# Performance work log

Measured on AMD Instinct MI355X. Metric: run time of the kernel, lower is better.

Reference implementation:

```python
import jax, jax.numpy as jnp
import numpy as np

B, T, D = 2, 2048, 1024
H = 16
HD = D // H  # head dim == config.k == config.v == 64


def setup_inputs() -> dict:
    key = jax.random.key(0)
    k1, k2, k3 = jax.random.split(key, 3)
    scale = 0.02
    x = jax.random.normal(k1, (B, T, D), dtype=jnp.float32)
    W1 = jax.random.normal(k2, (D, 3 * D), dtype=jnp.float32) * scale
    b1 = jnp.zeros((3 * D,), dtype=jnp.float32)
    W2 = jax.random.normal(k3, (D, D), dtype=jnp.float32) * scale
    b2 = jnp.zeros((D,), dtype=jnp.float32)
    return {"x": x, "W1": W1, "b1": b1, "W2": W2, "b2": b2}


def reference(x, W1, b1, W2, b2):
    # Fused QKV projection (dropout layers are identity in eval mode).
    Bx, Tx, C = x.shape
    qkv = x @ W1 + b1                      # [B, T, 3D]
    q, k, v = jnp.split(qkv, 3, axis=-1)   # each [B, T, D]
    q = q.reshape(Bx, Tx, H, HD).transpose(0, 2, 1, 3)  # [B, H, T, hd]
    k = k.reshape(Bx, Tx, H, HD).transpose(0, 2, 1, 3)
    v = v.reshape(Bx, Tx, H, HD).transpose(0, 2, 1, 3)

    logits = jnp.einsum('bhmk,bhnk->bhmn', q, k) / jnp.sqrt(jnp.float32(HD))
    # causal mask (lower-triangular bias buffer)
    causal = jnp.tril(jnp.ones((Tx, Tx), dtype=bool))
    logits = jnp.where(causal[None, None], logits, jnp.float32(-jnp.inf))
    att = jax.nn.softmax(logits, axis=-1)   # [B, H, T, T]

    y = jnp.einsum('bhmn,bhnv->bhmv', att, v)        # [B, H, T, hd]
    y = y.transpose(0, 2, 1, 3).reshape(Bx, Tx, C)   # [B, T, D]
    return y @ W2 + b2
```

## Files before the change

### kernel.cpp

```cpp
#include <hip/hip_runtime.h>

typedef __attribute__((ext_vector_type(8))) short bf16x8;
typedef __attribute__((ext_vector_type(4))) float f32x4;
typedef __attribute__((ext_vector_type(16))) float f32x16;
typedef __attribute__((ext_vector_type(4))) short short4v;
typedef __attribute__((ext_vector_type(4))) unsigned int uint4v;

#define B_  2
#define T_  2048
#define D_  1024
#define H_  16
#define HD_ 64

__device__ inline short f2bf(float f){
  unsigned u = __builtin_bit_cast(unsigned, f);
  u += 0x7fff + ((u >> 16) & 1);
  return (short)(u >> 16);
}

__device__ inline void gl2lds16(const void* g, void* l){
  __builtin_amdgcn_global_load_lds(
      (const __attribute__((address_space(1))) unsigned int*)g,
      (__attribute__((address_space(3))) unsigned int*)l, 16, 0, 0);
}

__global__ __launch_bounds__(256) void convert_f32_bf16(
    const float* __restrict__ in, short* __restrict__ out){
  int i = (blockIdx.x * 256 + threadIdx.x) * 4;
  float4 v = *(const float4*)(in + i);
  short4v o;
  o[0] = f2bf(v.x); o[1] = f2bf(v.y); o[2] = f2bf(v.z); o[3] = f2bf(v.w);
  *(short4v*)(out + i) = o;
}

__global__ __launch_bounds__(256) void transpose_f32_bf16(
    const float* __restrict__ in, short* __restrict__ out, int R, int C){
  __shared__ float tile[32][33];
  int tx = threadIdx.x & 31, ty0 = threadIdx.x >> 5;
  int bx = blockIdx.x << 5, by = blockIdx.y << 5;
#pragma unroll
  for (int i = 0; i < 4; i++){
    int ty = ty0 + i * 8;
    tile[ty][tx] = in[(by + ty) * C + bx + tx];
  }
  __syncthreads();
#pragma unroll
  for (int i = 0; i < 4; i++){
    int ty = ty0 + i * 8;
    out[(bx + ty) * R + by + tx] = f2bf(tile[tx][ty]);
  }
}

#define BM 128
#define BN 128
#define BK 32

#define QSCALE 0.18033688011112042f

template<int N_, int K_, int EPI>
__global__ __launch_bounds__(256) void gemm_bt(
    const short* __restrict__ A, const short* __restrict__ Bt,
    const float* __restrict__ bias,
    short* __restrict__ q, short* __restrict__ kk, short* __restrict__ vT,
    float* __restrict__ outf){
  __shared__ short As[2][BM * BK];
  __shared__ short Bs[2][BN * BK];
  const int tid = threadIdx.x;
  const int lane = tid & 63, w = tid >> 6;
  const int wm = w >> 1, wn = w & 1;
  const int lr = lane & 15, lk = lane >> 4;
  const int brow = blockIdx.y * BM, bcol = blockIdx.x * BN;
  f32x4 acc[4][4] = {};
  const short* Ag = A  + brow * K_;
  const short* Bg = Bt + bcol * K_;

  auto stage = [&](int buf, int k0){
#pragma unroll
    for (int i = 0; i < 2; i++){
      int idx = i * 256 + tid;
      int row = idx >> 2, c8 = (idx & 3) * 8;
      gl2lds16(Ag + row * K_ + k0 + c8, (char*)As[buf] + idx * 16);
      gl2lds16(Bg + row * K_ + k0 + c8, (char*)Bs[buf] + idx * 16);
    }
  };

  const int NT = K_ / BK;
  stage(0, 0);
  for (int t = 0; t < NT; ++t){
    const int cur = t & 1;
    if (t + 1 < NT){
      stage(cur ^ 1, (t + 1) * BK);
      asm volatile("s_waitcnt vmcnt(4)" ::: "memory");
    } else {
      asm volatile("s_waitcnt vmcnt(0)" ::: "memory");
    }
    __builtin_amdgcn_s_barrier();
    __builtin_amdgcn_sched_barrier(0);

    bf16x8 a[4], b[4];
#pragma unroll
    for (int mf = 0; mf < 4; mf++)
      a[mf] = *(const bf16x8*)(As[cur] + (wm * 64 + mf * 16 + lr) * BK + lk * 8);
#pragma unroll
    for (int nf = 0; nf < 4; nf++)
      b[nf] = *(const bf16x8*)(Bs[cur] + (wn * 64 + nf * 16 + lr) * BK + lk * 8);
    __builtin_amdgcn_s_setprio(1);
#pragma unroll
    for (int mf = 0; mf < 4; mf++)
#pragma unroll
      for (int nf = 0; nf < 4; nf++)
        acc[mf][nf] = __builtin_amdgcn_mfma_f32_16x16x32_bf16(a[mf], b[nf], acc[mf][nf], 0, 0, 0);
    __builtin_amdgcn_s_setprio(0);
    __builtin_amdgcn_sched_barrier(0);
    __builtin_amdgcn_s_barrier();
  }

  if constexpr (EPI == 0){
#pragma unroll
    for (int nf = 0; nf < 4; nf++){
      int n = bcol + wn * 64 + nf * 16 + lr;
      float bv = bias[n];
      int sec = n >> 10, d = n & 1023, h = d >> 6, hd = d & 63;
#pragma unroll
      for (int mf = 0; mf < 4; mf++){
        int m0 = brow + wm * 64 + mf * 16 + lk * 4;
        int b = m0 >> 11, t0 = m0 & 2047;
        int bh = b * H_ + h;
        if (sec == 0){
#pragma unroll
          for (int r = 0; r < 4; r++)
            q[(bh * T_ + t0 + r) * HD_ + hd] = f2bf((acc[mf][nf][r] + bv) * QSCALE);
        } else if (sec == 1){
#pragma unroll
          for (int r = 0; r < 4; r++)
            kk[(bh * T_ + t0 + r) * HD_ + hd] = f2bf(acc[mf][nf][r] + bv);
        } else {
          float v0 = acc[mf][nf][0] + bv, v1 = acc[mf][nf][1] + bv;
          float v2 = acc[mf][nf][2] + bv, v3 = acc[mf][nf][3] + bv;
          unsigned lo = (unsigned)(unsigned short)f2bf(v0) | ((unsigned)(unsigned short)f2bf(v1) << 16);
          unsigned hi = (unsigned)(unsigned short)f2bf(v2) | ((unsigned)(unsigned short)f2bf(v3) << 16);
          uint2 pk; pk.x = lo; pk.y = hi;
          *(uint2*)(vT + (bh * HD_ + hd) * T_ + t0) = pk;
        }
      }
    }
  } else {
#pragma unroll
    for (int nf = 0; nf < 4; nf++){
      int n = bcol + wn * 64 + nf * 16 + lr;
      float bv = bias[n];
#pragma unroll
      for (int mf = 0; mf < 4; mf++){
        int m0 = brow + wm * 64 + mf * 16 + lk * 4;
#pragma unroll
        for (int r = 0; r < 4; r++)
          outf[(m0 + r) * N_ + n] = acc[mf][nf][r] + bv;
      }
    }
  }
}

__global__ __launch_bounds__(256) void attn32(
    const short* __restrict__ Q, const short* __restrict__ Kg,
    const short* __restrict__ Vt, short* __restrict__ Y){
  __shared__ short Ks[2][64 * 64];
  __shared__ short Vs[2][64 * 64];
  __shared__ float bounce[4][32];
  const int tid = threadIdx.x;
  const int w = tid >> 6, l = tid & 63;
  const int lq = l & 31, h = l >> 5;
  const int bx = blockIdx.x;
  const int i = (bx < 256) ? 15 - (bx >> 5) : (bx >> 5) - 8;
  const int bh = bx & 31;
  const int q0 = i * 128, qw = q0 + w * 32;
  const int nt = 2 * (i + 1);

  bf16x8 qb[4];
  {
    const short* qbase = Q + (bh * T_ + qw + lq) * HD_;
#pragma unroll
    for (int dk = 0; dk < 4; dk++)
      qb[dk] = *(const bf16x8*)(qbase + dk * 16 + h * 8);
  }

  f32x16 o0 = {}, o1 = {};
  float m = -1e30f, ll = 0.f;

  auto stage = [&](int buf, int t){
#pragma unroll
    for (int j = 0; j < 2; j++){
      int idx = j * 256 + tid;
      int row = idx >> 3, cb = (idx & 7) * 16;
      int cbs = cb ^ ((row & 7) << 4);
      gl2lds16(Kg + (bh * T_ + t * 64 + row) * HD_ + (cbs >> 1), (char*)Ks[buf] + idx * 16);
      gl2lds16(Vt + (bh * HD_ + row) * T_ + t * 64 + (cbs >> 1), (char*)Vs[buf] + idx * 16);
    }
  };

  stage(0, 0);
  for (int t = 0; t < nt; ++t){
    const int cur = t & 1;
    if (t + 1 < nt){
      stage(cur ^ 1, t + 1);
      asm volatile("s_waitcnt vmcnt(4)" ::: "memory");
    } else {
      asm volatile("s_waitcnt vmcnt(0)" ::: "memory");
    }
    __builtin_amdgcn_s_barrier();
    __builtin_amdgcn_sched_barrier(0);

    const int kvb = t * 64;
    if (kvb <= qw + 31){
      const short* Kc = Ks[cur];
      const short* Vc = Vs[cur];

      f32x16 s[2] = {};
      __builtin_amdgcn_s_setprio(1);
#pragma unroll
      for (int kb = 0; kb < 2; kb++){
        int row = kb * 32 + lq;
        const char* rp = (const char*)Kc + row * 128;
        int swz = (row & 7) << 4;
#pragma unroll
        for (int dk = 0; dk < 4; dk++){
          bf16x8 ka = *(const bf16x8*)(rp + ((dk * 32 + h * 16) ^ swz));
          s[kb] = __builtin_amdgcn_mfma_f32_32x32x16_bf16(ka, qb[dk], s[kb], 0, 0, 0);
        }
      }
      __builtin_amdgcn_s_setprio(0);

      const int qg = qw + lq;
      if (kvb + 63 > qw){
#pragma unroll
        for (int kb = 0; kb < 2; kb++)
#pragma unroll
          for (int r = 0; r < 16; r++){
            int kv = kvb + kb * 32 + (r & 3) + 8 * (r >> 2) + 4 * h;
            if (kv > qg) s[kb][r] = -1e30f;
          }
      }

      float pm = s[0][0];
#pragma unroll
      for (int r = 1; r < 16; r++) pm = fmaxf(pm, s[0][r]);
#pragma unroll
      for (int r = 0; r < 16; r++) pm = fmaxf(pm, s[1][r]);
      pm = fmaxf(pm, __shfl_xor(pm, 32));

      if (__any(pm > m + 8.f)){
        float mn = fmaxf(pm, m);
        float sf = __builtin_amdgcn_exp2f(m - mn);
        m = mn;
        ll *= sf;
        bounce[w][lq] = sf;
#pragma unroll
        for (int r = 0; r < 16; r++){
          float sr = bounce[w][(r & 3) + 8 * (r >> 2) + 4 * h];
          o0[r] *= sr; o1[r] *= sr;
        }
      }

      float ts = 0.f;
#pragma unroll
      for (int kb = 0; kb < 2; kb++)
#pragma unroll
        for (int r = 0; r < 16; r++){
          float p = __builtin_amdgcn_exp2f(s[kb][r] - m);
          s[kb][r] = p;
          ts += p;
        }
      ts += __shfl_xor(ts, 32);
      ll += ts;

      unsigned pw0[8], pw1[8];
#pragma unroll
      for (int kb = 0; kb < 2; kb++)
#pragma unroll
        for (int gg = 0; gg < 4; gg++){
          unsigned r0, r1;
          asm("v_cvt_pk_bf16_f32 %0, %1, %2" : "=v"(r0) : "v"(s[kb][gg * 4 + 0]), "v"(s[kb][gg * 4 + 1]));
          asm("v_cvt_pk_bf16_f32 %0, %1, %2" : "=v"(r1) : "v"(s[kb][gg * 4 + 2]), "v"(s[kb][gg * 4 + 3]));
          pw0[kb * 4 + gg] = r0;
          pw1[kb * 4 + gg] = r1;
        }
#pragma unroll
      for (int ks = 0; ks < 4; ks++){
        asm("v_permlane32_swap_b32 %0, %1" : "+v"(pw0[2 * ks]), "+v"(pw0[2 * ks + 1]));
        asm("v_permlane32_swap_b32 %0, %1" : "+v"(pw1[2 * ks]), "+v"(pw1[2 * ks + 1]));
      }

      __builtin_amdgcn_s_setprio(1);
#pragma unroll
      for (int ks = 0; ks < 4; ks++){
        uint4v paw;
        paw[0] = pw0[2 * ks];     paw[1] = pw1[2 * ks];
        paw[2] = pw0[2 * ks + 1]; paw[3] = pw1[2 * ks + 1];
        bf16x8 pa = __builtin_bit_cast(bf16x8, paw);
#pragma unroll
        for (int nb = 0; nb < 2; nb++){
          int row = nb * 32 + lq;
          bf16x8 vb = *(const bf16x8*)((const char*)Vc + row * 128 +
                        ((ks * 32 + h * 16) ^ ((row & 7) << 4)));
          if (nb == 0) o0 = __builtin_amdgcn_mfma_f32_32x32x16_bf16(pa, vb, o0, 0, 0, 0);
          else         o1 = __builtin_amdgcn_mfma_f32_32x32x16_bf16(pa, vb, o1, 0, 0, 0);
        }
      }
      __builtin_amdgcn_s_setprio(0);
    }
    __builtin_amdgcn_sched_barrier(0);
    __builtin_amdgcn_s_barrier();
  }

  bounce[w][lq] = __builtin_amdgcn_rcpf(ll);
  const int b = bh >> 4, hh = bh & 15;
#pragma unroll
  for (int r = 0; r < 16; r++){
    int row = (r & 3) + 8 * (r >> 2) + 4 * h;
    float rl = bounce[w][row];
    int qg = qw + row;
    short* yb = Y + (b * T_ + qg) * D_ + hh * 64;
    yb[lq]      = f2bf(o0[r] * rl);
    yb[32 + lq] = f2bf(o1[r] * rl);
  }
}

extern "C" void kernel_launch(void* const* d_in, const int* in_sizes, int n_in,
                              void* d_out, int out_size, void* d_ws, size_t ws_size,
                              hipStream_t stream) {
  const float* x  = (const float*)d_in[0];
  const float* W1 = (const float*)d_in[1];
  const float* b1 = (const float*)d_in[2];
  const float* W2 = (const float*)d_in[3];
  const float* b2 = (const float*)d_in[4];
  float* out = (float*)d_out;

  char* ws = (char*)d_ws;
  short* W1T = (short*)(ws);
  short* W2T = (short*)(ws + 6291456);
  short* xb  = (short*)(ws + 8388608);
  short* q   = (short*)(ws + 16777216);
  short* kk  = (short*)(ws + 25165824);
  short* vT  = (short*)(ws + 33554432);
  short* y   = xb;

  convert_f32_bf16<<<dim3(4096), dim3(256), 0, stream>>>(x, xb);
  transpose_f32_bf16<<<dim3(96, 32), dim3(256), 0, stream>>>(W1, W1T, 1024, 3072);
  transpose_f32_bf16<<<dim3(32, 32), dim3(256), 0, stream>>>(W2, W2T, 1024, 1024);
  gemm_bt<3072, 1024, 0><<<dim3(24, 32), dim3(256), 0, stream>>>(xb, W1T, b1, q, kk, vT, nullptr);
  attn32<<<dim3(512), dim3(256), 0, stream>>>(q, kk, vT, y);
  gemm_bt<1024, 1024, 1><<<dim3(8, 32), dim3(256), 0, stream>>>(y, W2T, b2, nullptr, nullptr, nullptr, out);
}
```

Measured before the change: 130.3 us.

## Process two 64-key tiles per attention iteration with doubled LDS staging

The causal attention loop now handles 128 keys per iteration: each stage loads two 64-row K/V tiles into a doubled LDS buffer, and one online-softmax rescale covers both tiles. This halves the barrier and wait count and the number of max/rescale passes, and the max reduction is now a tree. In exchange LDS use doubles to 64KB per block, which may reduce occupancy, and register pressure rises from holding four score accumulators.

```diff
diff --git a/kernel.cpp b/kernel.cpp
--- a/kernel.cpp
+++ b/kernel.cpp
@@ -163,8 +163,8 @@
 __global__ __launch_bounds__(256) void attn32(
     const short* __restrict__ Q, const short* __restrict__ Kg,
     const short* __restrict__ Vt, short* __restrict__ Y){
-  __shared__ short Ks[2][64 * 64];
-  __shared__ short Vs[2][64 * 64];
+  __shared__ short Ks[2][2][64 * 64];
+  __shared__ short Vs[2][2][64 * 64];
   __shared__ float bounce[4][32];
   const int tid = threadIdx.x;
   const int w = tid >> 6, l = tid & 63;
@@ -173,7 +173,7 @@
   const int i = (bx < 256) ? 15 - (bx >> 5) : (bx >> 5) - 8;
   const int bh = bx & 31;
   const int q0 = i * 128, qw = q0 + w * 32;
-  const int nt = 2 * (i + 1);
+  const int np = i + 1;
 
   bf16x8 qb[4];
   {
@@ -186,127 +186,174 @@
   f32x16 o0 = {}, o1 = {};
   float m = -1e30f, ll = 0.f;
 
-  auto stage = [&](int buf, int t){
-#pragma unroll
-    for (int j = 0; j < 2; j++){
-      int idx = j * 256 + tid;
-      int row = idx >> 3, cb = (idx & 7) * 16;
-      int cbs = cb ^ ((row & 7) << 4);
-      gl2lds16(Kg + (bh * T_ + t * 64 + row) * HD_ + (cbs >> 1), (char*)Ks[buf] + idx * 16);
-      gl2lds16(Vt + (bh * HD_ + row) * T_ + t * 64 + (cbs >> 1), (char*)Vs[buf] + idx * 16);
+  auto stage = [&](int buf, int p){
+#pragma unroll
+    for (int s2 = 0; s2 < 2; s2++){
+      int t = 2 * p + s2;
+#pragma unroll
+      for (int j = 0; j < 2; j++){
+        int idx = j * 256 + tid;
+        int row = idx >> 3, cb = (idx & 7) * 16;
+        int cbs = cb ^ ((row & 7) << 4);
+        gl2lds16(Kg + (bh * T_ + t * 64 + row) * HD_ + (cbs >> 1), (char*)Ks[buf][s2] + idx * 16);
+        gl2lds16(Vt + (bh * HD_ + row) * T_ + t * 64 + (cbs >> 1), (char*)Vs[buf][s2] + idx * 16);
+      }
     }
   };
 
   stage(0, 0);
-  for (int t = 0; t < nt; ++t){
-    const int cur = t & 1;
-    if (t + 1 < nt){
-      stage(cur ^ 1, t + 1);
-      asm volatile("s_waitcnt vmcnt(4)" ::: "memory");
+  for (int p = 0; p < np; ++p){
+    const int cur = p & 1;
+    if (p + 1 < np){
+      stage(cur ^ 1, p + 1);
+      asm volatile("s_waitcnt vmcnt(8)" ::: "memory");
     } else {
       asm volatile("s_waitcnt vmcnt(0)" ::: "memory");
     }
     __builtin_amdgcn_s_barrier();
     __builtin_amdgcn_sched_barrier(0);
 
-    const int kvb = t * 64;
-    if (kvb <= qw + 31){
-      const short* Kc = Ks[cur];
-      const short* Vc = Vs[cur];
-
-      f32x16 s[2] = {};
-      __builtin_amdgcn_s_setprio(1);
+    const int kvb0 = p * 128;
+    const bool act1 = (kvb0 + 64 <= qw + 31);
+    const int qg = qw + lq;
+
+    f32x16 s4[4] = {};
+    __builtin_amdgcn_s_setprio(1);
+#pragma unroll
+    for (int kb = 0; kb < 2; kb++){
+      int row = kb * 32 + lq;
+      const char* rp = (const char*)Ks[cur][0] + row * 128;
+      int swz = (row & 7) << 4;
+#pragma unroll
+      for (int dk = 0; dk < 4; dk++){
+        bf16x8 ka = *(const bf16x8*)(rp + ((dk * 32 + h * 16) ^ swz));
+        s4[kb] = __builtin_amdgcn_mfma_f32_32x32x16_bf16(ka, qb[dk], s4[kb], 0, 0, 0);
+      }
+    }
+    if (act1){
 #pragma unroll
       for (int kb = 0; kb < 2; kb++){
         int row = kb * 32 + lq;
-        const char* rp = (const char*)Kc + row * 128;
+        const char* rp = (const char*)Ks[cur][1] + row * 128;
         int swz = (row & 7) << 4;
 #pragma unroll
         for (int dk = 0; dk < 4; dk++){
           bf16x8 ka = *(const bf16x8*)(rp + ((dk * 32 + h * 16) ^ swz));
-          s[kb] = __builtin_amdgcn_mfma_f32_32x32x16_bf16(ka, qb[dk], s[kb], 0, 0, 0);
-        }
-      }
-      __builtin_amdgcn_s_setprio(0);
-
-      const int qg = qw + lq;
-      if (kvb + 63 > qw){
+          s4[2 + kb] = __builtin_amdgcn_mfma_f32_32x32x16_bf16(ka, qb[dk], s4[2 + kb], 0, 0, 0);
+        }
+      }
+    }
+    __builtin_amdgcn_s_setprio(0);
+
+    if (kvb0 + 63 > qw){
+#pragma unroll
+      for (int kb = 0; kb < 2; kb++)
+#pragma unroll
+        for (int r = 0; r < 16; r++){
+          int kv = kvb0 + kb * 32 + (r & 3) + 8 * (r >> 2) + 4 * h;
+          if (kv > qg) s4[kb][r] = -1e30f;
+        }
+    }
+    if (act1 && kvb0 + 127 > qw){
+#pragma unroll
+      for (int kb = 0; kb < 2; kb++)
+#pragma unroll
+        for (int r = 0; r < 16; r++){
+          int kv = kvb0 + 64 + kb * 32 + (r & 3) + 8 * (r >> 2) + 4 * h;
+          if (kv > qg) s4[2 + kb][r] = -1e30f;
+        }
+    }
+
+    float vm[16];
+#pragma unroll
+    for (int r = 0; r < 16; r++) vm[r] = fmaxf(s4[0][r], s4[1][r]);
+    if (act1){
+#pragma unroll
+      for (int r = 0; r < 16; r++) vm[r] = fmaxf(vm[r], fmaxf(s4[2][r], s4[3][r]));
+    }
+#pragma unroll
+    for (int st = 8; st > 0; st >>= 1)
+#pragma unroll
+      for (int r = 0; r < st; r++) vm[r] = fmaxf(vm[r], vm[r + st]);
+    float pm = fmaxf(vm[0], __shfl_xor(vm[0], 32));
+
+    if (__any(pm > m + 8.f)){
+      float mn = fmaxf(pm, m);
+      float sf = __builtin_amdgcn_exp2f(m - mn);
+      m = mn;
+      ll *= sf;
+      bounce[w][lq] = sf;
+#pragma unroll
+      for (int r = 0; r < 16; r++){
+        float sr = bounce[w][(r & 3) + 8 * (r >> 2) + 4 * h];
+        o0[r] *= sr; o1[r] *= sr;
+      }
+    }
+
+    float ts = 0.f;
+#pragma unroll
+    for (int kb = 0; kb < 2; kb++)
+#pragma unroll
+      for (int r = 0; r < 16; r++){
+        float pv = __builtin_amdgcn_exp2f(s4[kb][r] - m);
+        s4[kb][r] = pv;
+        ts += pv;
+      }
+    if (act1){
+#pragma unroll
+      for (int kb = 2; kb < 4; kb++)
+#pragma unroll
+        for (int r = 0; r < 16; r++){
+          float pv = __builtin_amdgcn_exp2f(s4[kb][r] - m);
+          s4[kb][r] = pv;
+          ts += pv;
+        }
+    }
+    ts += __shfl_xor(ts, 32);
+    ll += ts;
+
+#pragma unroll
+    for (int s2 = 0; s2 < 2; s2++){
+      if (s2 == 0 || act1){
+        unsigned pw0[8], pw1[8];
 #pragma unroll
         for (int kb = 0; kb < 2; kb++)
 #pragma unroll
-          for (int r = 0; r < 16; r++){
-            int kv = kvb + kb * 32 + (r & 3) + 8 * (r >> 2) + 4 * h;
-            if (kv > qg) s[kb][r] = -1e30f;
+          for (int gg = 0; gg < 4; gg++){
+            unsigned r0, r1;
+            asm("v_cvt_pk_bf16_f32 %0, %1, %2" : "=v"(r0)
+                : "v"(s4[s2 * 2 + kb][gg * 4 + 0]), "v"(s4[s2 * 2 + kb][gg * 4 + 1]));
+            asm("v_cvt_pk_bf16_f32 %0, %1, %2" : "=v"(r1)
+                : "v"(s4[s2 * 2 + kb][gg * 4 + 2]), "v"(s4[s2 * 2 + kb][gg * 4 + 3]));
+            pw0[kb * 4 + gg] = r0;
+            pw1[kb * 4 + gg] = r1;
           }
-      }
-
-      float pm = s[0][0];
-#pragma unroll
-      for (int r = 1; r < 16; r++) pm = fmaxf(pm, s[0][r]);
-#pragma unroll
-      for (int r = 0; r < 16; r++) pm = fmaxf(pm, s[1][r]);
-      pm = fmaxf(pm, __shfl_xor(pm, 32));
-
-      if (__any(pm > m + 8.f)){
-        float mn = fmaxf(pm, m);
-        float sf = __builtin_amdgcn_exp2f(m - mn);
-        m = mn;
-        ll *= sf;
-        bounce[w][lq] = sf;
-#pragma unroll
-        for (int r = 0; r < 16; r++){
-          float sr = bounce[w][(r & 3) + 8 * (r >> 2) + 4 * h];
-          o0[r] *= sr; o1[r] *= sr;
-        }
-      }
-
-      float ts = 0.f;
-#pragma unroll
-      for (int kb = 0; kb < 2; kb++)
-#pragma unroll
-        for (int r = 0; r < 16; r++){
-          float p = __builtin_amdgcn_exp2f(s[kb][r] - m);
-          s[kb][r] = p;
-          ts += p;
-        }
-      ts += __shfl_xor(ts, 32);
-      ll += ts;
-
-      unsigned pw0[8], pw1[8];
-#pragma unroll
-      for (int kb = 0; kb < 2; kb++)
-#pragma unroll
-        for (int gg = 0; gg < 4; gg++){
-          unsigned r0, r1;
-          asm("v_cvt_pk_bf16_f32 %0, %1, %2" : "=v"(r0) : "v"(s[kb][gg * 4 + 0]), "v"(s[kb][gg * 4 + 1]));
-          asm("v_cvt_pk_bf16_f32 %0, %1, %2" : "=v"(r1) : "v"(s[kb][gg * 4 + 2]), "v"(s[kb][gg * 4 + 3]));
-          pw0[kb * 4 + gg] = r0;
-          pw1[kb * 4 + gg] = r1;
-        }
-#pragma unroll
-      for (int ks = 0; ks < 4; ks++){
-        asm("v_permlane32_swap_b32 %0, %1" : "+v"(pw0[2 * ks]), "+v"(pw0[2 * ks + 1]));
-        asm("v_permlane32_swap_b32 %0, %1" : "+v"(pw1[2 * ks]), "+v"(pw1[2 * ks + 1]));
-      }
-
-      __builtin_amdgcn_s_setprio(1);
-#pragma unroll
-      for (int ks = 0; ks < 4; ks++){
-        uint4v paw;
-        paw[0] = pw0[2 * ks];     paw[1] = pw1[2 * ks];
-        paw[2] = pw0[2 * ks + 1]; paw[3] = pw1[2 * ks + 1];
-        bf16x8 pa = __builtin_bit_cast(bf16x8, paw);
-#pragma unroll
-        for (int nb = 0; nb < 2; nb++){
-          int row = nb * 32 + lq;
-          bf16x8 vb = *(const bf16x8*)((const char*)Vc + row * 128 +
-                        ((ks * 32 + h * 16) ^ ((row & 7) << 4)));
-          if (nb == 0) o0 = __builtin_amdgcn_mfma_f32_32x32x16_bf16(pa, vb, o0, 0, 0, 0);
-          else         o1 = __builtin_amdgcn_mfma_f32_32x32x16_bf16(pa, vb, o1, 0, 0, 0);
-        }
-      }
-      __builtin_amdgcn_s_setprio(0);
-    }
+#pragma unroll
+        for (int ks = 0; ks < 4; ks++){
+          asm("v_permlane32_swap_b32 %0, %1" : "+v"(pw0[2 * ks]), "+v"(pw0[2 * ks + 1]));
+          asm("v_permlane32_swap_b32 %0, %1" : "+v"(pw1[2 * ks]), "+v"(pw1[2 * ks + 1]));
+        }
+
+        __builtin_amdgcn_s_setprio(1);
+#pragma unroll
+        for (int ks = 0; ks < 4; ks++){
+          uint4v paw;
+          paw[0] = pw0[2 * ks];     paw[1] = pw1[2 * ks];
+          paw[2] = pw0[2 * ks + 1]; paw[3] = pw1[2 * ks + 1];
+          bf16x8 pa = __builtin_bit_cast(bf16x8, paw);
+#pragma unroll
+          for (int nb = 0; nb < 2; nb++){
+            int row = nb * 32 + lq;
+            bf16x8 vb = *(const bf16x8*)((const char*)Vs[cur][s2] + row * 128 +
+                          ((ks * 32 + h * 16) ^ ((row & 7) << 4)));
+            if (nb == 0) o0 = __builtin_amdgcn_mfma_f32_32x32x16_bf16(pa, vb, o0, 0, 0, 0);
+            else         o1 = __builtin_amdgcn_mfma_f32_32x32x16_bf16(pa, vb, o1, 0, 0, 0);
+          }
+        }
+        __builtin_amdgcn_s_setprio(0);
+      }
+    }
+
     __builtin_amdgcn_sched_barrier(0);
     __builtin_amdgcn_s_barrier();
   }
```

New measurement: 140.4 us. 7.8% more time.

## Split attention KV range across two blocks and merge partial softmax results

Applied to the files above, without the earlier changes.

Each query tile's KV loop is split into two halves processed by separate blocks (1024 blocks instead of 512). Each block writes unnormalized fp32 partial outputs plus running max and sum, and a new merge kernel combines them into the bf16 output. This is meant to raise parallelism and occupancy on the 256-CU device, since 512 uneven blocks underfill it. The cost is an extra kernel launch and roughly 34MB of fp32 partials written and read back. The split path only runs when the workspace is large enough.

```diff
diff --git a/kernel.cpp b/kernel.cpp
--- a/kernel.cpp
+++ b/kernel.cpp
@@ -160,9 +160,13 @@
   }
 }
 
-__global__ __launch_bounds__(256) void attn32(
+__device__ inline int crow(int r, int h){ return (r & 3) + 8 * (r >> 2) + 4 * h; }
+
+template<int SPLIT>
+__global__ __launch_bounds__(256, 4) void attn32(
     const short* __restrict__ Q, const short* __restrict__ Kg,
-    const short* __restrict__ Vt, short* __restrict__ Y){
+    const short* __restrict__ Vt, short* __restrict__ Y,
+    float* __restrict__ Op, float* __restrict__ ml){
   __shared__ short Ks[2][64 * 64];
   __shared__ short Vs[2][64 * 64];
   __shared__ float bounce[4][32];
@@ -170,10 +174,19 @@
   const int w = tid >> 6, l = tid & 63;
   const int lq = l & 31, h = l >> 5;
   const int bx = blockIdx.x;
-  const int i = (bx < 256) ? 15 - (bx >> 5) : (bx >> 5) - 8;
+  int i, hf;
+  if constexpr (SPLIT){
+    int u = bx >> 5, v = u & 15;
+    i = (v < 8) ? 15 - v : v - 8;
+    hf = u >> 4;
+  } else {
+    i = (bx < 256) ? 15 - (bx >> 5) : (bx >> 5) - 8;
+    hf = 0;
+  }
   const int bh = bx & 31;
   const int q0 = i * 128, qw = q0 + w * 32;
-  const int nt = 2 * (i + 1);
+  const int t0 = (SPLIT && hf) ? (i + 1) : 0;
+  const int t1 = (SPLIT && !hf) ? (i + 1) : 2 * (i + 1);
 
   bf16x8 qb[4];
   {
@@ -197,10 +210,10 @@
     }
   };
 
-  stage(0, 0);
-  for (int t = 0; t < nt; ++t){
-    const int cur = t & 1;
-    if (t + 1 < nt){
+  stage(0, t0);
+  for (int t = t0; t < t1; ++t){
+    const int cur = (t - t0) & 1;
+    if (t + 1 < t1){
       stage(cur ^ 1, t + 1);
       asm volatile("s_waitcnt vmcnt(4)" ::: "memory");
     } else {
@@ -235,7 +248,7 @@
         for (int kb = 0; kb < 2; kb++)
 #pragma unroll
           for (int r = 0; r < 16; r++){
-            int kv = kvb + kb * 32 + (r & 3) + 8 * (r >> 2) + 4 * h;
+            int kv = kvb + kb * 32 + crow(r, h);
             if (kv > qg) s[kb][r] = -1e30f;
           }
       }
@@ -255,7 +268,7 @@
         bounce[w][lq] = sf;
 #pragma unroll
         for (int r = 0; r < 16; r++){
-          float sr = bounce[w][(r & 3) + 8 * (r >> 2) + 4 * h];
+          float sr = bounce[w][crow(r, h)];
           o0[r] *= sr; o1[r] *= sr;
         }
       }
@@ -311,16 +324,58 @@
     __builtin_amdgcn_s_barrier();
   }
 
-  bounce[w][lq] = __builtin_amdgcn_rcpf(ll);
-  const int b = bh >> 4, hh = bh & 15;
-#pragma unroll
-  for (int r = 0; r < 16; r++){
-    int row = (r & 3) + 8 * (r >> 2) + 4 * h;
-    float rl = bounce[w][row];
-    int qg = qw + row;
-    short* yb = Y + (b * T_ + qg) * D_ + hh * 64;
-    yb[lq]      = f2bf(o0[r] * rl);
-    yb[32 + lq] = f2bf(o1[r] * rl);
+  if constexpr (SPLIT){
+    float* Oq = Op + ((size_t)(hf * 32 + bh)) * (size_t)T_ * 64;
+    if (h == 0){
+      float* mlr = ml + ((size_t)(hf * 32 + bh) * T_ + (qw + lq)) * 2;
+      mlr[0] = m; mlr[1] = ll;
+    }
+#pragma unroll
+    for (int r = 0; r < 16; r++){
+      int qg = qw + crow(r, h);
+      Oq[qg * 64 + lq]      = o0[r];
+      Oq[qg * 64 + 32 + lq] = o1[r];
+    }
+  } else {
+    bounce[w][lq] = __builtin_amdgcn_rcpf(ll);
+    const int b = bh >> 4, hh = bh & 15;
+#pragma unroll
+    for (int r = 0; r < 16; r++){
+      int row = crow(r, h);
+      float rl = bounce[w][row];
+      int qg = qw + row;
+      short* yb = Y + (b * T_ + qg) * D_ + hh * 64;
+      yb[lq]      = f2bf(o0[r] * rl);
+      yb[32 + lq] = f2bf(o1[r] * rl);
+    }
+  }
+}
+
+__global__ __launch_bounds__(256) void attn_merge(
+    const float* __restrict__ Op, const float* __restrict__ ml,
+    short* __restrict__ Y){
+  int gid = blockIdx.x * 256 + threadIdx.x;
+  int rid = gid >> 2, c16 = (gid & 3) * 16;
+  float m1 = ml[rid * 2],           l1 = ml[rid * 2 + 1];
+  float m2 = ml[131072 + rid * 2],  l2 = ml[131072 + rid * 2 + 1];
+  float M  = fmaxf(m1, m2);
+  float f1 = __builtin_amdgcn_exp2f(m1 - M);
+  float f2 = __builtin_amdgcn_exp2f(m2 - M);
+  float rl = 1.f / (f1 * l1 + f2 * l2);
+  f1 *= rl; f2 *= rl;
+  const float4* O1 = (const float4*)(Op + (size_t)rid * 64 + c16);
+  const float4* O2 = (const float4*)(Op + 4194304ull + (size_t)rid * 64 + c16);
+  int bh = rid >> 11, t = rid & 2047;
+  short* yb = Y + (((bh >> 4) * T_ + t) * D_) + (bh & 15) * 64 + c16;
+#pragma unroll
+  for (int j = 0; j < 4; j++){
+    float4 a = O1[j], b = O2[j];
+    short4v o;
+    o[0] = f2bf(f1 * a.x + f2 * b.x);
+    o[1] = f2bf(f1 * a.y + f2 * b.y);
+    o[2] = f2bf(f1 * a.z + f2 * b.z);
+    o[3] = f2bf(f1 * a.w + f2 * b.w);
+    *(short4v*)(yb + j * 4) = o;
   }
 }
 
@@ -341,12 +396,22 @@
   short* q   = (short*)(ws + 16777216);
   short* kk  = (short*)(ws + 25165824);
   short* vT  = (short*)(ws + 33554432);
+  float* Op  = (float*)(ws + 41943040);
+  float* mlb = (float*)(ws + 41943040 + 33554432);
   short* y   = xb;
+
+  const size_t need = 41943040ull + 33554432ull + 1048576ull;
+  const bool split = ws_size >= need;
 
   convert_f32_bf16<<<dim3(4096), dim3(256), 0, stream>>>(x, xb);
   transpose_f32_bf16<<<dim3(96, 32), dim3(256), 0, stream>>>(W1, W1T, 1024, 3072);
   transpose_f32_bf16<<<dim3(32, 32), dim3(256), 0, stream>>>(W2, W2T, 1024, 1024);
   gemm_bt<3072, 1024, 0><<<dim3(24, 32), dim3(256), 0, stream>>>(xb, W1T, b1, q, kk, vT, nullptr);
-  attn32<<<dim3(512), dim3(256), 0, stream>>>(q, kk, vT, y);
+  if (split){
+    attn32<1><<<dim3(1024), dim3(256), 0, stream>>>(q, kk, vT, nullptr, Op, mlb);
+    attn_merge<<<dim3(1024), dim3(256), 0, stream>>>(Op, mlb, y);
+  } else {
+    attn32<0><<<dim3(512), dim3(256), 0, stream>>>(q, kk, vT, y, nullptr, nullptr);
+  }
   gemm_bt<1024, 1024, 1><<<dim3(8, 32), dim3(256), 0, stream>>>(y, W2T, b2, nullptr, nullptr, nullptr, out);
 }
```

Result: faster. 123.4 us (-5.3%).
